# Kernel optimization log

Measured on AMD Instinct MI355X. Metric: run time of the kernel, lower is better.

The kernel has to match this reference:

```python
import jax, jax.numpy as jnp
import numpy as np

B, S = 2, 1024          # 2 sequences of 1024 tokens (prefill)
HID = 2880
HQ, HKV, D = 64, 8, 64  # query heads, kv heads, head_dim
W = 128                 # sliding window size
THETA = 150000.0
SCALE = D ** -0.5
Q_SIZE, KV_SIZE = HQ * D, HKV * D


def _rope_neox(pos, x):
    # pos: [T] int, x: [T, H, D] -> neox-style full-dim rotary
    half = D // 2
    inv_freq = 1.0 / (THETA ** (jnp.arange(half, dtype=jnp.float32) * 2.0 / D))
    ang = pos.astype(jnp.float32)[:, None] * inv_freq          # [T, D/2]
    cos = jnp.cos(ang)[:, None, :]                             # [T, 1, D/2]
    sin = jnp.sin(ang)[:, None, :]
    x1, x2 = x[..., :half], x[..., half:]
    return jnp.concatenate([x1 * cos - x2 * sin, x1 * sin + x2 * cos], axis=-1)


def setup_inputs() -> dict:
    key = jax.random.key(0)
    ks = jax.random.split(key, 10)
    s = 0.02
    hidden_states = jax.random.normal(ks[0], (B * S, HID), dtype=jnp.float32)
    positions = jnp.tile(jnp.arange(S, dtype=jnp.int32), B)    # per-sequence positions
    Wq = jax.random.normal(ks[1], (HID, Q_SIZE), dtype=jnp.float32) * s
    bq = jax.random.normal(ks[2], (Q_SIZE,), dtype=jnp.float32) * s
    Wk = jax.random.normal(ks[3], (HID, KV_SIZE), dtype=jnp.float32) * s
    bk = jax.random.normal(ks[4], (KV_SIZE,), dtype=jnp.float32) * s
    Wv = jax.random.normal(ks[5], (HID, KV_SIZE), dtype=jnp.float32) * s
    bv = jax.random.normal(ks[6], (KV_SIZE,), dtype=jnp.float32) * s
    Wo = jax.random.normal(ks[7], (Q_SIZE, HID), dtype=jnp.float32) * s
    bo = jax.random.normal(ks[8], (HID,), dtype=jnp.float32) * s
    return {"hidden_states": hidden_states, "positions": positions,
            "Wq": Wq, "bq": bq, "Wk": Wk, "bk": bk,
            "Wv": Wv, "bv": bv, "Wo": Wo, "bo": bo}


def reference(hidden_states, positions, Wq, bq, Wk, bk, Wv, bv, Wo, bo):
    T = hidden_states.shape[0]
    q = (hidden_states @ Wq + bq).reshape(T, HQ, D)
    k = (hidden_states @ Wk + bk).reshape(T, HKV, D)
    v = (hidden_states @ Wv + bv).reshape(T, HKV, D)
    q = _rope_neox(positions, q)
    k = _rope_neox(positions, k)

    # sliding-window causal attention (banded, window = last W keys + self)
    G = HQ // HKV  # GQA group size
    q5 = q.reshape(B, S, HKV, G, D)
    k4 = k.reshape(B, S, HKV, D)
    v4 = v.reshape(B, S, HKV, D)
    offs = jnp.arange(W + 1)
    idx = jnp.arange(S)[:, None] - W + offs[None, :]           # [S, W+1] key index j
    valid = idx >= 0                                           # causal+window band
    idx_c = jnp.clip(idx, 0, S - 1)
    kw = k4[:, idx_c]                                          # [B, S, W+1, HKV, D]
    vw = v4[:, idx_c]
    scores = jnp.einsum('bikgd,biwkd->bikgw', q5, kw) * SCALE  # [B,S,HKV,G,W+1]
    scores = jnp.where(valid[None, :, None, None, :], scores, jnp.float32(-1e30))
    p = jax.nn.softmax(scores, axis=-1)
    o = jnp.einsum('bikgw,biwkd->bikgd', p, vw).reshape(T, Q_SIZE)
    return o @ Wo + bo


if __name__ == '__main__':
    out = reference(**setup_inputs())
    print(out.shape, out.dtype)
```

## Files before the change

kernel.cpp:

```cpp
#include <hip/hip_runtime.h>

#define T_TOK 2048
#define S_LEN 1024
#define HIDN  2880
#define NHQ   64
#define NHKV  8
#define DH    64
#define QSZ   4096
#define KVSZ  512
#define WIN   128
#define NQKV  5120
#define NOPAD 2944

typedef __attribute__((ext_vector_type(4))) float f32x4;
typedef __attribute__((ext_vector_type(8))) short bf16x8;
typedef __attribute__((ext_vector_type(4))) short s16x4;

__device__ __forceinline__ unsigned short f2bf(float f) {
  unsigned u = __float_as_uint(f);
  u += 0x7fffu + ((u >> 16) & 1u);
  return (unsigned short)(u >> 16);
}
__device__ __forceinline__ float bf2f(unsigned short s) {
  return __uint_as_float(((unsigned)s) << 16);
}
__device__ __forceinline__ void ld_g2l16(const void* g, void* l) {
  __builtin_amdgcn_global_load_lds(
      (const __attribute__((address_space(1))) unsigned int*)g,
      (__attribute__((address_space(3))) unsigned int*)l, 16, 0, 0);
}

#define NB_CONV 2880
#define NB_WQ   5760
#define NB_WK   720

__device__ __forceinline__ void transpose_tile(
    const float* __restrict__ W, unsigned short* __restrict__ WT,
    int N, int lbid, float (*tile)[72])
{
  const int tid = threadIdx.x;
  const int nbx = N >> 6;
  const int nb = (lbid % nbx) * 64;
  const int kb = (lbid / nbx) * 32;
  const int kk = tid >> 3;
  const int n8 = (tid & 7) * 8;
  const float* src = W + (size_t)(kb + kk) * N + nb + n8;
  *(f32x4*)&tile[kk][n8]     = *(const f32x4*)(src);
  *(f32x4*)&tile[kk][n8 + 4] = *(const f32x4*)(src + 4);
  __syncthreads();
  const int n  = tid & 63;
  const int k8 = (tid >> 6) * 8;
  bf16x8 p;
  #pragma unroll
  for (int j = 0; j < 8; ++j) p[j] = (short)f2bf(tile[k8 + j][n]);
  *(bf16x8*)(WT + (size_t)(nb + n) * HIDN + kb + k8) = p;
}

__global__ __launch_bounds__(256) void prep_kernel(
    const float* __restrict__ hidden, unsigned short* __restrict__ hbf,
    const float* __restrict__ Wq, const float* __restrict__ Wk,
    const float* __restrict__ Wv, unsigned short* __restrict__ WT)
{
  __shared__ float tile[32][72];
  const int bid = blockIdx.x;
  if (bid < NB_CONV) {
    const size_t off = ((size_t)bid * 256 + threadIdx.x) * 8;
    const f32x4 a = *(const f32x4*)(hidden + off);
    const f32x4 b = *(const f32x4*)(hidden + off + 4);
    bf16x8 p;
    p[0] = (short)f2bf(a[0]); p[1] = (short)f2bf(a[1]);
    p[2] = (short)f2bf(a[2]); p[3] = (short)f2bf(a[3]);
    p[4] = (short)f2bf(b[0]); p[5] = (short)f2bf(b[1]);
    p[6] = (short)f2bf(b[2]); p[7] = (short)f2bf(b[3]);
    *(bf16x8*)(hbf + off) = p;
  } else if (bid < NB_CONV + NB_WQ) {
    transpose_tile(Wq, WT, QSZ, bid - NB_CONV, tile);
  } else if (bid < NB_CONV + NB_WQ + NB_WK) {
    transpose_tile(Wk, WT + (size_t)QSZ * HIDN, KVSZ,
                   bid - NB_CONV - NB_WQ, tile);
  } else {
    transpose_tile(Wv, WT + (size_t)(QSZ + KVSZ) * HIDN, KVSZ,
                   bid - NB_CONV - NB_WQ - NB_WK, tile);
  }
}

__global__ __launch_bounds__(256) void transpose_w(
    const float* __restrict__ W, unsigned short* __restrict__ WT,
    int K, int N)
{
  __shared__ float tile[32][72];
  const int tid = threadIdx.x;
  const int nb = blockIdx.x * 64;
  const int kb = blockIdx.y * 32;
  const int kk = tid >> 3;
  const int n8 = (tid & 7) * 8;
  if (nb + 64 <= N) {
    const float* src = W + (size_t)(kb + kk) * N + nb + n8;
    *(f32x4*)&tile[kk][n8]     = *(const f32x4*)(src);
    *(f32x4*)&tile[kk][n8 + 4] = *(const f32x4*)(src + 4);
  } else {
    #pragma unroll
    for (int u = 0; u < 8; ++u)
      tile[kk][n8 + u] = (nb + n8 + u < N)
          ? W[(size_t)(kb + kk) * N + nb + n8 + u] : 0.f;
  }
  __syncthreads();
  const int n  = tid & 63;
  const int k8 = (tid >> 6) * 8;
  bf16x8 p;
  #pragma unroll
  for (int j = 0; j < 8; ++j) p[j] = (short)f2bf(tile[k8 + j][n]);
  *(bf16x8*)(WT + (size_t)(nb + n) * K + kb + k8) = p;
}

__device__ __forceinline__ void rope_epilogue(
    f32x4 acc[4][4], const float* __restrict__ bias,
    const int* __restrict__ pos, unsigned short* __restrict__ outp,
    int outStride, int colbase, int rowbase, int lane)
{
  const int fr = lane & 15;
  const int r4 = (lane >> 4) * 4;
  const float invf0 = exp2f((float)fr        * (-17.19460283f / 32.0f));
  const float invf1 = exp2f((float)(fr + 16) * (-17.19460283f / 32.0f));
  #pragma unroll
  for (int mt = 0; mt < 4; ++mt) {
    #pragma unroll
    for (int i = 0; i < 4; ++i) {
      const int m = rowbase + mt * 16 + r4 + i;
      const float p = (float)pos[m];
      #pragma unroll
      for (int ntp = 0; ntp < 2; ++ntp) {
        float sv, cv;
        __sincosf(p * (ntp ? invf1 : invf0), &sv, &cv);
        const int c1 = colbase + ntp * 16 + fr;
        const float x1 = acc[mt][ntp][i]     + bias[c1];
        const float x2 = acc[mt][ntp + 2][i] + bias[c1 + 32];
        outp[(size_t)m * outStride + c1]      = f2bf(x1 * cv - x2 * sv);
        outp[(size_t)m * outStride + c1 + 32] = f2bf(x1 * sv + x2 * cv);
      }
    }
  }
}

__global__ __launch_bounds__(128) void gemm_qkv(
    const unsigned short* __restrict__ A, const unsigned short* __restrict__ BT,
    const float* __restrict__ bq, const float* __restrict__ bk,
    const float* __restrict__ bv, const int* __restrict__ pos,
    unsigned short* __restrict__ qb, unsigned short* __restrict__ kb,
    unsigned short* __restrict__ vT)
{
  __shared__ unsigned short As[64 * 64];
  __shared__ unsigned short Bs[128 * 64];
  const int tid  = threadIdx.x;
  const int lane = tid & 63;
  const int wid  = tid >> 6;
  const int m0 = blockIdx.y * 64;
  const int n0 = blockIdx.x * 128;
  const int wn = wid * 64;
  const int fr = lane & 15;
  const int fq = lane >> 4;

  f32x4 acc[4][4];
  #pragma unroll
  for (int i = 0; i < 4; ++i)
    #pragma unroll
    for (int j = 0; j < 4; ++j) acc[i][j] = (f32x4){0.f, 0.f, 0.f, 0.f};

  const int rsub = tid >> 3;
  const int cg   = (tid & 7) ^ (rsub & 7);
  const unsigned short* Ap = A  + (size_t)(m0 + rsub) * HIDN + cg * 8;
  const unsigned short* Bp = BT + (size_t)(n0 + rsub) * HIDN + cg * 8;
  const size_t rstep = (size_t)16 * HIDN;

  for (int k0 = 0; k0 < HIDN; k0 += 64) {
    #pragma unroll
    for (int i = 0; i < 4; ++i)
      ld_g2l16(Ap + i * rstep + k0, As + ((size_t)i * 128 + tid) * 8);
    #pragma unroll
    for (int i = 0; i < 8; ++i)
      ld_g2l16(Bp + i * rstep + k0, Bs + ((size_t)i * 128 + tid) * 8);
    __syncthreads();
    #pragma unroll
    for (int ks = 0; ks < 2; ++ks) {
      const int kc = ks * 4 + fq;
      bf16x8 af[4], bfr[4];
      #pragma unroll
      for (int mt = 0; mt < 4; ++mt) {
        const int R = mt * 16 + fr;
        af[mt] = *(const bf16x8*)(As + R * 64 + ((kc ^ (R & 7)) << 3));
      }
      #pragma unroll
      for (int nt = 0; nt < 4; ++nt) {
        const int R = wn + nt * 16 + fr;
        bfr[nt] = *(const bf16x8*)(Bs + R * 64 + ((kc ^ (R & 7)) << 3));
      }
      #pragma unroll
      for (int mt = 0; mt < 4; ++mt)
        #pragma unroll
        for (int nt = 0; nt < 4; ++nt)
          acc[mt][nt] = __builtin_amdgcn_mfma_f32_16x16x32_bf16(
              af[mt], bfr[nt], acc[mt][nt], 0, 0, 0);
    }
    __syncthreads();
  }

  const int r4 = (lane >> 4) * 4;
  if (n0 < QSZ) {
    rope_epilogue(acc, bq, pos, qb, QSZ, n0 + wn, m0, lane);
  } else if (n0 < QSZ + KVSZ) {
    rope_epilogue(acc, bk, pos, kb, KVSZ, n0 - QSZ + wn, m0, lane);
  } else {
    #pragma unroll
    for (int nt = 0; nt < 4; ++nt) {
      const int vrow = n0 - (QSZ + KVSZ) + wn + nt * 16 + fr;
      const float bvv = bv[vrow];
      #pragma unroll
      for (int mt = 0; mt < 4; ++mt) {
        const int mb = m0 + mt * 16 + r4;
        s16x4 p;
        p[0] = (short)f2bf(acc[mt][nt][0] + bvv);
        p[1] = (short)f2bf(acc[mt][nt][1] + bvv);
        p[2] = (short)f2bf(acc[mt][nt][2] + bvv);
        p[3] = (short)f2bf(acc[mt][nt][3] + bvv);
        *(s16x4*)(vT + (size_t)vrow * T_TOK + mb) = p;
      }
    }
  }
}

__global__ __launch_bounds__(128) void gemm_o(
    const unsigned short* __restrict__ A, const unsigned short* __restrict__ BT,
    const float* __restrict__ bias, float* __restrict__ C)
{
  __shared__ unsigned short As[64 * 64];
  __shared__ unsigned short Bs[128 * 64];
  const int tid  = threadIdx.x;
  const int lane = tid & 63;
  const int wid  = tid >> 6;
  const int m0 = blockIdx.y * 64;
  const int n0 = blockIdx.x * 128;
  const int wn = wid * 64;
  const int fr = lane & 15;
  const int fq = lane >> 4;

  f32x4 acc[4][4];
  #pragma unroll
  for (int i = 0; i < 4; ++i)
    #pragma unroll
    for (int j = 0; j < 4; ++j) acc[i][j] = (f32x4){0.f, 0.f, 0.f, 0.f};

  const int rsub = tid >> 3;
  const int cg   = (tid & 7) ^ (rsub & 7);
  const unsigned short* Ap = A  + (size_t)(m0 + rsub) * QSZ + cg * 8;
  const unsigned short* Bp = BT + (size_t)(n0 + rsub) * QSZ + cg * 8;
  const size_t rstep = (size_t)16 * QSZ;

  for (int k0 = 0; k0 < QSZ; k0 += 64) {
    #pragma unroll
    for (int i = 0; i < 4; ++i)
      ld_g2l16(Ap + i * rstep + k0, As + ((size_t)i * 128 + tid) * 8);
    #pragma unroll
    for (int i = 0; i < 8; ++i)
      ld_g2l16(Bp + i * rstep + k0, Bs + ((size_t)i * 128 + tid) * 8);
    __syncthreads();
    #pragma unroll
    for (int ks = 0; ks < 2; ++ks) {
      const int kc = ks * 4 + fq;
      bf16x8 af[4], bfr[4];
      #pragma unroll
      for (int mt = 0; mt < 4; ++mt) {
        const int R = mt * 16 + fr;
        af[mt] = *(const bf16x8*)(As + R * 64 + ((kc ^ (R & 7)) << 3));
      }
      #pragma unroll
      for (int nt = 0; nt < 4; ++nt) {
        const int R = wn + nt * 16 + fr;
        bfr[nt] = *(const bf16x8*)(Bs + R * 64 + ((kc ^ (R & 7)) << 3));
      }
      #pragma unroll
      for (int mt = 0; mt < 4; ++mt)
        #pragma unroll
        for (int nt = 0; nt < 4; ++nt)
          acc[mt][nt] = __builtin_amdgcn_mfma_f32_16x16x32_bf16(
              af[mt], bfr[nt], acc[mt][nt], 0, 0, 0);
    }
    __syncthreads();
  }

  const int r4 = (lane >> 4) * 4;
  #pragma unroll
  for (int nt = 0; nt < 4; ++nt) {
    const int n = n0 + wn + nt * 16 + fr;
    if (n >= HIDN) continue;
    const float bvv = bias[n];
    #pragma unroll
    for (int mt = 0; mt < 4; ++mt) {
      const int mb = m0 + mt * 16 + r4;
      #pragma unroll
      for (int i = 0; i < 4; ++i)
        C[(size_t)(mb + i) * HIDN + n] = acc[mt][nt][i] + bvv;
    }
  }
}

__global__ __launch_bounds__(256, 3) void attn_kernel(
    const unsigned short* __restrict__ q, const unsigned short* __restrict__ k,
    const unsigned short* __restrict__ vT, unsigned short* __restrict__ o)
{
  __shared__ unsigned short lds[26624];
  unsigned short* Ks = lds;
  unsigned short* Vt = lds;
  unsigned short* Ps = lds + 13824;

  const int tid  = threadIdx.x;
  const int lane = tid & 63;
  const int wid  = tid >> 6;
  const int sq0  = blockIdx.x * 64;
  const int hp   = blockIdx.y;
  const int b    = blockIdx.z;
  const int h0   = hp * 2;
  const int kvh  = hp >> 2;
  const int kp0  = sq0 - WIN;

  const int fr = lane & 15;
  const int fk = (lane >> 4) * 8;
  const int qw = wid * 16;

  bf16x8 qf[2][2];
  {
    const size_t qrow = (size_t)(b * S_LEN + sq0 + qw + fr) * QSZ;
    #pragma unroll
    for (int hh = 0; hh < 2; ++hh)
      #pragma unroll
      for (int ks2 = 0; ks2 < 2; ++ks2)
        qf[hh][ks2] = *(const bf16x8*)(q + qrow + (h0 + hh) * DH + ks2 * 32 + fk);
  }

  #pragma unroll
  for (int j = 0; j < 6; ++j) {
    const int c  = tid + j * 256;
    const int kr = c >> 3, dc = (c & 7) * 8;
    int tok = b * S_LEN + kp0 + kr;
    if (tok < 0) tok = 0;
    const bf16x8 vv = *(const bf16x8*)(k + (size_t)tok * KVSZ + kvh * DH + dc);
    *(bf16x8*)&Ks[kr * 72 + dc] = vv;
  }
  __syncthreads();

  f32x4 S0[12], S1[12];
  #pragma unroll
  for (int i = 0; i < 12; ++i) {
    S0[i] = (f32x4){0.f, 0.f, 0.f, 0.f};
    S1[i] = (f32x4){0.f, 0.f, 0.f, 0.f};
  }
  #pragma unroll
  for (int ks2 = 0; ks2 < 2; ++ks2) {
    #pragma unroll
    for (int nt = 0; nt < 12; ++nt) {
      const bf16x8 bfr = *(const bf16x8*)&Ks[(nt * 16 + fr) * 72 + ks2 * 32 + fk];
      S0[nt] = __builtin_amdgcn_mfma_f32_16x16x32_bf16(qf[0][ks2], bfr, S0[nt], 0, 0, 0);
      S1[nt] = __builtin_amdgcn_mfma_f32_16x16x32_bf16(qf[1][ks2], bfr, S1[nt], 0, 0, 0);
    }
  }

  const int qbase = sq0 + qw + ((lane >> 4) << 2);
  float ls0[4] = {0.f, 0.f, 0.f, 0.f};
  float ls1[4] = {0.f, 0.f, 0.f, 0.f};
  #pragma unroll
  for (int nt = 0; nt < 12; ++nt) {
    const int jpos = kp0 + nt * 16 + fr;
    #pragma unroll
    for (int i = 0; i < 4; ++i) {
      const int qa = qbase + i;
      const bool valid = (jpos >= 0) && (jpos <= qa) && (jpos >= qa - WIN);
      const float e0 = valid ? __expf(S0[nt][i] * 0.125f) : 0.f;
      const float e1 = valid ? __expf(S1[nt][i] * 0.125f) : 0.f;
      S0[nt][i] = e0; ls0[i] += e0;
      S1[nt][i] = e1; ls1[i] += e1;
    }
  }
  #pragma unroll
  for (int off = 1; off < 16; off <<= 1)
    #pragma unroll
    for (int i = 0; i < 4; ++i) {
      ls0[i] += __shfl_xor(ls0[i], off, 64);
      ls1[i] += __shfl_xor(ls1[i], off, 64);
    }
  float inv0[4], inv1[4];
  #pragma unroll
  for (int i = 0; i < 4; ++i) {
    inv0[i] = 1.0f / ls0[i];
    inv1[i] = 1.0f / ls1[i];
  }
  __syncthreads();

  #pragma unroll
  for (int nt = 0; nt < 12; ++nt)
    #pragma unroll
    for (int i = 0; i < 4; ++i)
      Ps[(qbase - sq0 + i) * 200 + nt * 16 + fr] = f2bf(S0[nt][i]);
  if (kp0 >= 0) {
    #pragma unroll
    for (int j = 0; j < 6; ++j) {
      const int c  = tid + j * 256;
      const int dr = c / 24, kc = (c % 24) * 8;
      const bf16x8 vv = *(const bf16x8*)(
          vT + (size_t)(kvh * DH + dr) * T_TOK + b * S_LEN + kp0 + kc);
      *(bf16x8*)&Vt[dr * 200 + kc] = vv;
    }
  } else {
    #pragma unroll
    for (int j = 0; j < 6; ++j) {
      const int c  = tid + j * 256;
      const int dr = c / 24, kc = (c % 24) * 8;
      bf16x8 vv;
      #pragma unroll
      for (int u = 0; u < 8; ++u) {
        int col = b * S_LEN + kp0 + kc + u;
        if (col < 0) col = 0;
        vv[u] = (short)vT[(size_t)(kvh * DH + dr) * T_TOK + col];
      }
      *(bf16x8*)&Vt[dr * 200 + kc] = vv;
    }
  }
  __syncthreads();

  {
    f32x4 O[4];
    #pragma unroll
    for (int i = 0; i < 4; ++i) O[i] = (f32x4){0.f, 0.f, 0.f, 0.f};
    #pragma unroll
    for (int ks2 = 0; ks2 < 6; ++ks2) {
      const bf16x8 pa = *(const bf16x8*)&Ps[(qw + fr) * 200 + ks2 * 32 + fk];
      #pragma unroll
      for (int nt = 0; nt < 4; ++nt) {
        const bf16x8 vb = *(const bf16x8*)&Vt[(nt * 16 + fr) * 200 + ks2 * 32 + fk];
        O[nt] = __builtin_amdgcn_mfma_f32_16x16x32_bf16(pa, vb, O[nt], 0, 0, 0);
      }
    }
    #pragma unroll
    for (int nt = 0; nt < 4; ++nt)
      #pragma unroll
      for (int i = 0; i < 4; ++i)
        o[(size_t)(b * S_LEN + qbase + i) * QSZ + h0 * DH + nt * 16 + fr] =
            f2bf(O[nt][i] * inv0[i]);
  }
  __syncthreads();

  #pragma unroll
  for (int nt = 0; nt < 12; ++nt)
    #pragma unroll
    for (int i = 0; i < 4; ++i)
      Ps[(qbase - sq0 + i) * 200 + nt * 16 + fr] = f2bf(S1[nt][i]);
  __syncthreads();

  {
    f32x4 O[4];
    #pragma unroll
    for (int i = 0; i < 4; ++i) O[i] = (f32x4){0.f, 0.f, 0.f, 0.f};
    #pragma unroll
    for (int ks2 = 0; ks2 < 6; ++ks2) {
      const bf16x8 pa = *(const bf16x8*)&Ps[(qw + fr) * 200 + ks2 * 32 + fk];
      #pragma unroll
      for (int nt = 0; nt < 4; ++nt) {
        const bf16x8 vb = *(const bf16x8*)&Vt[(nt * 16 + fr) * 200 + ks2 * 32 + fk];
        O[nt] = __builtin_amdgcn_mfma_f32_16x16x32_bf16(pa, vb, O[nt], 0, 0, 0);
      }
    }
    #pragma unroll
    for (int nt = 0; nt < 4; ++nt)
      #pragma unroll
      for (int i = 0; i < 4; ++i)
        o[(size_t)(b * S_LEN + qbase + i) * QSZ + (h0 + 1) * DH + nt * 16 + fr] =
            f2bf(O[nt][i] * inv1[i]);
  }
}

extern "C" void kernel_launch(void* const* d_in, const int* in_sizes, int n_in,
                              void* d_out, int out_size, void* d_ws, size_t ws_size,
                              hipStream_t stream) {
  const float* hidden    = (const float*)d_in[0];
  const int*   positions = (const int*)d_in[1];
  const float* Wq = (const float*)d_in[2];
  const float* bq = (const float*)d_in[3];
  const float* Wk = (const float*)d_in[4];
  const float* bk = (const float*)d_in[5];
  const float* Wv = (const float*)d_in[6];
  const float* bv = (const float*)d_in[7];
  const float* Wo = (const float*)d_in[8];
  const float* bo = (const float*)d_in[9];
  float* out = (float*)d_out;

  char* ws = (char*)d_ws;
  unsigned short* hbf   = (unsigned short*)(ws);
  unsigned short* WqkvT = (unsigned short*)(ws + 11796480);
  unsigned short* qb    = (unsigned short*)(ws + 41287680);
  unsigned short* kb    = (unsigned short*)(ws + 58064896);
  unsigned short* vTb   = (unsigned short*)(ws + 60162048);

  prep_kernel<<<dim3(NB_CONV + NB_WQ + 2 * NB_WK), dim3(256), 0, stream>>>(
      hidden, hbf, Wq, Wk, Wv, WqkvT);

  gemm_qkv<<<dim3(NQKV / 128, T_TOK / 64), dim3(128), 0, stream>>>(
      hbf, WqkvT, bq, bk, bv, positions, qb, kb, vTb);

  transpose_w<<<dim3(NOPAD / 64, QSZ / 32), dim3(256), 0, stream>>>(
      Wo, WqkvT, QSZ, HIDN);

  attn_kernel<<<dim3(S_LEN / 64, NHQ / 2, 2), dim3(256), 0, stream>>>(
      qb, kb, vTb, qb);
  gemm_o<<<dim3(NOPAD / 128, T_TOK / 64), dim3(128), 0, stream>>>(
      qb, WqkvT, bo, out);
}
```

Measured before the change: 385.4 us.

## Double-buffer LDS tiles in QKV and output GEMMs with K-step 32

Both GEMM kernels now keep two LDS buffers of half-width K tiles (32 instead of 64). The load of the next tile is issued right after the barrier, while MFMAs run on the current tile, and there is one barrier per iteration instead of two. The aim is to hide global-to-LDS load latency behind compute. In exchange there are twice as many loop iterations, and the XOR swizzle is narrower (4 slots), which may cause more LDS bank conflicts.

```diff
diff --git a/kernel.cpp b/kernel.cpp
--- a/kernel.cpp
+++ b/kernel.cpp
@@ -149,8 +149,8 @@
     unsigned short* __restrict__ qb, unsigned short* __restrict__ kb,
     unsigned short* __restrict__ vT)
 {
-  __shared__ unsigned short As[64 * 64];
-  __shared__ unsigned short Bs[128 * 64];
+  __shared__ unsigned short As[2][64 * 32];
+  __shared__ unsigned short Bs[2][128 * 32];
   const int tid  = threadIdx.x;
   const int lane = tid & 63;
   const int wid  = tid >> 6;
@@ -166,42 +166,46 @@
     #pragma unroll
     for (int j = 0; j < 4; ++j) acc[i][j] = (f32x4){0.f, 0.f, 0.f, 0.f};
 
-  const int rsub = tid >> 3;
-  const int cg   = (tid & 7) ^ (rsub & 7);
+  const int rsub  = tid >> 2;
+  const int cslot = tid & 3;
+  const int cg    = cslot ^ (rsub & 3);
   const unsigned short* Ap = A  + (size_t)(m0 + rsub) * HIDN + cg * 8;
   const unsigned short* Bp = BT + (size_t)(n0 + rsub) * HIDN + cg * 8;
-  const size_t rstep = (size_t)16 * HIDN;
-
-  for (int k0 = 0; k0 < HIDN; k0 += 64) {
+  const size_t rstep = (size_t)32 * HIDN;
+
+  auto stage = [&](int b, int k0) {
+    #pragma unroll
+    for (int i = 0; i < 2; ++i)
+      ld_g2l16(Ap + i * rstep + k0, &As[b][i * 1024 + tid * 8]);
     #pragma unroll
     for (int i = 0; i < 4; ++i)
-      ld_g2l16(Ap + i * rstep + k0, As + ((size_t)i * 128 + tid) * 8);
-    #pragma unroll
-    for (int i = 0; i < 8; ++i)
-      ld_g2l16(Bp + i * rstep + k0, Bs + ((size_t)i * 128 + tid) * 8);
+      ld_g2l16(Bp + i * rstep + k0, &Bs[b][i * 1024 + tid * 8]);
+  };
+
+  stage(0, 0);
+  const int NIT = HIDN / 32;
+  for (int it = 0; it < NIT; ++it) {
     __syncthreads();
-    #pragma unroll
-    for (int ks = 0; ks < 2; ++ks) {
-      const int kc = ks * 4 + fq;
-      bf16x8 af[4], bfr[4];
-      #pragma unroll
-      for (int mt = 0; mt < 4; ++mt) {
-        const int R = mt * 16 + fr;
-        af[mt] = *(const bf16x8*)(As + R * 64 + ((kc ^ (R & 7)) << 3));
-      }
-      #pragma unroll
-      for (int nt = 0; nt < 4; ++nt) {
-        const int R = wn + nt * 16 + fr;
-        bfr[nt] = *(const bf16x8*)(Bs + R * 64 + ((kc ^ (R & 7)) << 3));
-      }
-      #pragma unroll
-      for (int mt = 0; mt < 4; ++mt)
-        #pragma unroll
-        for (int nt = 0; nt < 4; ++nt)
-          acc[mt][nt] = __builtin_amdgcn_mfma_f32_16x16x32_bf16(
-              af[mt], bfr[nt], acc[mt][nt], 0, 0, 0);
-    }
-    __syncthreads();
+    if (it + 1 < NIT) stage((it + 1) & 1, (it + 1) * 32);
+    const unsigned short* as = As[it & 1];
+    const unsigned short* bs = Bs[it & 1];
+    bf16x8 af[4], bfr[4];
+    #pragma unroll
+    for (int mt = 0; mt < 4; ++mt) {
+      const int R = mt * 16 + fr;
+      af[mt] = *(const bf16x8*)(as + R * 32 + ((fq ^ (R & 3)) << 3));
+    }
+    #pragma unroll
+    for (int nt = 0; nt < 4; ++nt) {
+      const int R = wn + nt * 16 + fr;
+      bfr[nt] = *(const bf16x8*)(bs + R * 32 + ((fq ^ (R & 3)) << 3));
+    }
+    #pragma unroll
+    for (int mt = 0; mt < 4; ++mt)
+      #pragma unroll
+      for (int nt = 0; nt < 4; ++nt)
+        acc[mt][nt] = __builtin_amdgcn_mfma_f32_16x16x32_bf16(
+            af[mt], bfr[nt], acc[mt][nt], 0, 0, 0);
   }
 
   const int r4 = (lane >> 4) * 4;
@@ -232,8 +236,8 @@
     const unsigned short* __restrict__ A, const unsigned short* __restrict__ BT,
     const float* __restrict__ bias, float* __restrict__ C)
 {
-  __shared__ unsigned short As[64 * 64];
-  __shared__ unsigned short Bs[128 * 64];
+  __shared__ unsigned short As[2][64 * 32];
+  __shared__ unsigned short Bs[2][128 * 32];
   const int tid  = threadIdx.x;
   const int lane = tid & 63;
   const int wid  = tid >> 6;
@@ -249,42 +253,46 @@
     #pragma unroll
     for (int j = 0; j < 4; ++j) acc[i][j] = (f32x4){0.f, 0.f, 0.f, 0.f};
 
-  const int rsub = tid >> 3;
-  const int cg   = (tid & 7) ^ (rsub & 7);
+  const int rsub  = tid >> 2;
+  const int cslot = tid & 3;
+  const int cg    = cslot ^ (rsub & 3);
   const unsigned short* Ap = A  + (size_t)(m0 + rsub) * QSZ + cg * 8;
   const unsigned short* Bp = BT + (size_t)(n0 + rsub) * QSZ + cg * 8;
-  const size_t rstep = (size_t)16 * QSZ;
-
-  for (int k0 = 0; k0 < QSZ; k0 += 64) {
+  const size_t rstep = (size_t)32 * QSZ;
+
+  auto stage = [&](int b, int k0) {
+    #pragma unroll
+    for (int i = 0; i < 2; ++i)
+      ld_g2l16(Ap + i * rstep + k0, &As[b][i * 1024 + tid * 8]);
     #pragma unroll
     for (int i = 0; i < 4; ++i)
-      ld_g2l16(Ap + i * rstep + k0, As + ((size_t)i * 128 + tid) * 8);
-    #pragma unroll
-    for (int i = 0; i < 8; ++i)
-      ld_g2l16(Bp + i * rstep + k0, Bs + ((size_t)i * 128 + tid) * 8);
+      ld_g2l16(Bp + i * rstep + k0, &Bs[b][i * 1024 + tid * 8]);
+  };
+
+  stage(0, 0);
+  const int NIT = QSZ / 32;
+  for (int it = 0; it < NIT; ++it) {
     __syncthreads();
-    #pragma unroll
-    for (int ks = 0; ks < 2; ++ks) {
-      const int kc = ks * 4 + fq;
-      bf16x8 af[4], bfr[4];
-      #pragma unroll
-      for (int mt = 0; mt < 4; ++mt) {
-        const int R = mt * 16 + fr;
-        af[mt] = *(const bf16x8*)(As + R * 64 + ((kc ^ (R & 7)) << 3));
-      }
-      #pragma unroll
-      for (int nt = 0; nt < 4; ++nt) {
-        const int R = wn + nt * 16 + fr;
-        bfr[nt] = *(const bf16x8*)(Bs + R * 64 + ((kc ^ (R & 7)) << 3));
-      }
-      #pragma unroll
-      for (int mt = 0; mt < 4; ++mt)
-        #pragma unroll
-        for (int nt = 0; nt < 4; ++nt)
-          acc[mt][nt] = __builtin_amdgcn_mfma_f32_16x16x32_bf16(
-              af[mt], bfr[nt], acc[mt][nt], 0, 0, 0);
-    }
-    __syncthreads();
+    if (it + 1 < NIT) stage((it + 1) & 1, (it + 1) * 32);
+    const unsigned short* as = As[it & 1];
+    const unsigned short* bs = Bs[it & 1];
+    bf16x8 af[4], bfr[4];
+    #pragma unroll
+    for (int mt = 0; mt < 4; ++mt) {
+      const int R = mt * 16 + fr;
+      af[mt] = *(const bf16x8*)(as + R * 32 + ((fq ^ (R & 3)) << 3));
+    }
+    #pragma unroll
+    for (int nt = 0; nt < 4; ++nt) {
+      const int R = wn + nt * 16 + fr;
+      bfr[nt] = *(const bf16x8*)(bs + R * 32 + ((fq ^ (R & 3)) << 3));
+    }
+    #pragma unroll
+    for (int mt = 0; mt < 4; ++mt)
+      #pragma unroll
+      for (int nt = 0; nt < 4; ++nt)
+        acc[mt][nt] = __builtin_amdgcn_mfma_f32_16x16x32_bf16(
+            af[mt], bfr[nt], acc[mt][nt], 0, 0, 0);
   }
 
   const int r4 = (lane >> 4) * 4;
```

Result: slower. 461.9 us (+19.8%).
